# Kernel optimization log

Measured on AMD Instinct MI355X. Metric: run time of the kernel, lower is better.

Reference implementation:

```python
import jax, jax.numpy as jnp
from jax import lax
import numpy as np

N_BITS = 108
N_OUT = 7
# pos_bits[i, j] = bit j (MSB-first) of index i, matching `i >> (6 - j) & 1`
POS_BITS = np.array([[(i >> (6 - j)) & 1 for j in range(N_OUT)] for i in range(N_BITS)], dtype=np.float32)
# LZC value when all 108 bits are zero: 108 = 1101100b, MSB first
LZC_108 = np.array([1, 1, 0, 1, 1, 0, 0], dtype=np.float32)


def setup_inputs() -> dict:
    key = jax.random.key(0)
    # sparse binary bits so leading-zero runs are long and some rows are all-zero
    X = (jax.random.uniform(key, (2_000_000, N_BITS)) < 0.03).astype(jnp.float32)
    return {"X": X}


def _lzd(X):
    """X: [..., 108] MSB-first bits -> [..., 7] LZC MSB-first.

    Arithmetic soft-gate semantics: NOT(a)=1-a, AND(a,b)=a*b,
    OR(a,b)=a+b-a*b, MUX(s,a,b)=s*a+(1-s)*b, OR-tree = 1-prod(1-x).
    Sequential carry over `found` expressed with lax.scan (108 steps).
    """
    batch_shape = X.shape[:-1]
    bits = jnp.moveaxis(X, -1, 0)  # [108, ...]
    pos = jnp.asarray(POS_BITS, dtype=X.dtype)  # [108, 7]

    def step(carry, inp):
        found, lzc = carry                  # found: [..., 1], lzc: [..., 7]
        bit, pos_bits = inp                 # bit: [...], pos_bits: [7]
        bit = bit[..., None]                # [..., 1]
        not_found = 1.0 - found             # NOT
        is_first = bit * not_found          # AND
        # MUX per output bit: is_first ? pos_bit : lzc
        lzc = is_first * pos_bits + (1.0 - is_first) * lzc
        # OR: found | is_first
        found = found + is_first - found * is_first
        return (found, lzc), None

    found0 = jnp.zeros(batch_shape + (1,), X.dtype)
    lzc0 = jnp.zeros(batch_shape + (N_OUT,), X.dtype)
    (found, lzc), _ = lax.scan(step, (found0, lzc0), (bits, pos))

    # OR-tree over all 108 bits, then all-zero override with LZC=108
    any_one = 1.0 - jnp.prod(1.0 - X, axis=-1, keepdims=True)  # [..., 1]
    all_zero = 1.0 - any_one                                   # NOT
    lzc108 = jnp.asarray(LZC_108, dtype=X.dtype)               # [7]
    return all_zero * lzc108 + (1.0 - all_zero) * lzc


def reference(X):
    return _lzd(X)
```

## Files before the change

kernel.cpp:

```cpp
#include <hip/hip_runtime.h>


#define NBITS 108
#define NOUT 7
#define F4R 27

__global__ __launch_bounds__(256) void lzd108_kernel(const uint4* __restrict__ X4,
                                                     float* __restrict__ out,
                                                     int n_rows) {
    const int lane = threadIdx.x & 63;
    const long long wave    = (long long)blockIdx.x * 4 + (threadIdx.x >> 6);
    const long long nwaves  = (long long)gridDim.x * 4;
    const long long ngroups = ((long long)n_rows + 3) >> 2;

    for (long long g = wave; g < ngroups; g += nwaves) {
        const long long row0 = g << 2;
        int rows_here = (int)(n_rows - row0);
        if (rows_here > 4) rows_here = 4;
        const int act0 = (rows_here >= 2 ? 2 : rows_here) * F4R;
        const int act1 = (rows_here > 2 ? rows_here - 2 : 0) * F4R;

        const uint4* base = X4 + row0 * F4R;
        unsigned m0 = 0u, m1 = 0u;
        if (lane < act0) {
            uint4 v = base[lane];
            m0 = (v.x ? 1u : 0u) | (v.y ? 2u : 0u) | (v.z ? 4u : 0u) | (v.w ? 8u : 0u);
        }
        if (lane < act1) {
            uint4 v = base[54 + lane];
            m1 = (v.x ? 1u : 0u) | (v.y ? 2u : 0u) | (v.z ? 4u : 0u) | (v.w ? 8u : 0u);
        }
        const unsigned long long nz0 = __ballot(m0 != 0u);
        const unsigned long long nz1 = __ballot(m1 != 0u);

        int i0 = NBITS, i1 = NBITS, i2 = NBITS, i3 = NBITS;
        {
            const unsigned long long a = nz0 & 0x7FFFFFFull;
            if (a) { const int l = __ffsll(a) - 1;
                     const unsigned mm = __builtin_amdgcn_readlane(m0, l);
                     i0 = l * 4 + __ffs(mm) - 1; }
            const unsigned long long b = (nz0 >> 27) & 0x7FFFFFFull;
            if (b) { const int l = __ffsll(b) - 1;
                     const unsigned mm = __builtin_amdgcn_readlane(m0, l + 27);
                     i1 = l * 4 + __ffs(mm) - 1; }
            const unsigned long long c = nz1 & 0x7FFFFFFull;
            if (c) { const int l = __ffsll(c) - 1;
                     const unsigned mm = __builtin_amdgcn_readlane(m1, l);
                     i2 = l * 4 + __ffs(mm) - 1; }
            const unsigned long long d = (nz1 >> 27) & 0x7FFFFFFull;
            if (d) { const int l = __ffsll(d) - 1;
                     const unsigned mm = __builtin_amdgcn_readlane(m1, l + 27);
                     i3 = l * 4 + __ffs(mm) - 1; }
        }

        if (lane < NOUT * rows_here) {
            const int r = lane / NOUT;
            const int j = lane - r * NOUT;
            const int id01 = (r == 0) ? i0 : i1;
            const int id23 = (r == 2) ? i2 : i3;
            const int id = (r < 2) ? id01 : id23;
            out[row0 * NOUT + lane] = (float)((id >> (6 - j)) & 1);
        }
    }
}

extern "C" void kernel_launch(void* const* d_in, const int* in_sizes, int n_in,
                              void* d_out, int out_size, void* d_ws, size_t ws_size,
                              hipStream_t stream) {
    const uint4* X4 = (const uint4*)d_in[0];
    float* out = (float*)d_out;
    const int n_rows = in_sizes[0] / NBITS;
    const int grid = 4096;
    lzd108_kernel<<<grid, 256, 0, stream>>>(X4, out, n_rows);
}
```

Before: 1.095 ms.

## Scan 8 rows per wave, reading only each row's leading bits first

Each wave now handles 8 rows. It first loads only the first 32 bits (8 uint4) of each row and reads the remaining 76 bits only for rows whose prefix is all zero, batching up to 3 such rows per follow-up load. Because the inputs are sparse, this is meant to skip most of the 432 bytes per row that were previously read, cutting HBM traffic. Outputs are packed and written as float4. The trade-offs are data-dependent branching, serial follow-up loops and scattered partial-row reads that may waste cache-line bandwidth.

```diff
diff --git a/kernel.cpp b/kernel.cpp
--- a/kernel.cpp
+++ b/kernel.cpp
@@ -11,55 +11,99 @@
     const int lane = threadIdx.x & 63;
     const long long wave    = (long long)blockIdx.x * 4 + (threadIdx.x >> 6);
     const long long nwaves  = (long long)gridDim.x * 4;
-    const long long ngroups = ((long long)n_rows + 3) >> 2;
+    const long long ngroups = ((long long)n_rows + 7) >> 3;
+
+    const int r8  = lane >> 3;
+    const int k8  = lane & 7;
+    const int rr  = lane / 19;
+    const int k19 = lane - rr * 19;
 
     for (long long g = wave; g < ngroups; g += nwaves) {
-        const long long row0 = g << 2;
+        const long long row0 = g << 3;
         int rows_here = (int)(n_rows - row0);
-        if (rows_here > 4) rows_here = 4;
-        const int act0 = (rows_here >= 2 ? 2 : rows_here) * F4R;
-        const int act1 = (rows_here > 2 ? rows_here - 2 : 0) * F4R;
+        if (rows_here > 8) rows_here = 8;
+        const uint4* base = X4 + row0 * F4R;
 
-        const uint4* base = X4 + row0 * F4R;
-        unsigned m0 = 0u, m1 = 0u;
-        if (lane < act0) {
-            uint4 v = base[lane];
-            m0 = (v.x ? 1u : 0u) | (v.y ? 2u : 0u) | (v.z ? 4u : 0u) | (v.w ? 8u : 0u);
-        }
-        if (lane < act1) {
-            uint4 v = base[54 + lane];
-            m1 = (v.x ? 1u : 0u) | (v.y ? 2u : 0u) | (v.z ? 4u : 0u) | (v.w ? 8u : 0u);
-        }
-        const unsigned long long nz0 = __ballot(m0 != 0u);
-        const unsigned long long nz1 = __ballot(m1 != 0u);
+        if (rows_here == 8) {
+            uint4 v = base[r8 * F4R + k8];
+            unsigned m = (v.x ? 1u : 0u) | (v.y ? 2u : 0u)
+                       | (v.z ? 4u : 0u) | (v.w ? 8u : 0u);
+            const unsigned long long nz = __ballot(m != 0u);
 
-        int i0 = NBITS, i1 = NBITS, i2 = NBITS, i3 = NBITS;
-        {
-            const unsigned long long a = nz0 & 0x7FFFFFFull;
-            if (a) { const int l = __ffsll(a) - 1;
-                     const unsigned mm = __builtin_amdgcn_readlane(m0, l);
-                     i0 = l * 4 + __ffs(mm) - 1; }
-            const unsigned long long b = (nz0 >> 27) & 0x7FFFFFFull;
-            if (b) { const int l = __ffsll(b) - 1;
-                     const unsigned mm = __builtin_amdgcn_readlane(m0, l + 27);
-                     i1 = l * 4 + __ffs(mm) - 1; }
-            const unsigned long long c = nz1 & 0x7FFFFFFull;
-            if (c) { const int l = __ffsll(c) - 1;
-                     const unsigned mm = __builtin_amdgcn_readlane(m1, l);
-                     i2 = l * 4 + __ffs(mm) - 1; }
-            const unsigned long long d = (nz1 >> 27) & 0x7FFFFFFull;
-            if (d) { const int l = __ffsll(d) - 1;
-                     const unsigned mm = __builtin_amdgcn_readlane(m1, l + 27);
-                     i3 = l * 4 + __ffs(mm) - 1; }
-        }
+            unsigned long long packed = 0;
+            unsigned long long list = 0;
+            int nu = 0;
+            #pragma unroll
+            for (int r = 0; r < 8; ++r) {
+                const unsigned g8 = (unsigned)(nz >> (8 * r)) & 0xFFu;
+                if (g8) {
+                    const int l = __ffs(g8) - 1;
+                    const unsigned mm = __builtin_amdgcn_readlane(m, 8 * r + l);
+                    const unsigned id = 4u * l + __ffs(mm) - 1u;
+                    packed |= (unsigned long long)id << (7 * r);
+                } else {
+                    list |= (unsigned long long)r << (4 * nu);
+                    ++nu;
+                }
+            }
 
-        if (lane < NOUT * rows_here) {
-            const int r = lane / NOUT;
-            const int j = lane - r * NOUT;
-            const int id01 = (r == 0) ? i0 : i1;
-            const int id23 = (r == 2) ? i2 : i3;
-            const int id = (r < 2) ? id01 : id23;
-            out[row0 * NOUT + lane] = (float)((id >> (6 - j)) & 1);
+            int done = 0;
+            while (done < nu) {
+                int take = nu - done;
+                if (take > 3) take = 3;
+                unsigned m2 = 0u;
+                const bool active = (lane < 19 * take);
+                if (active) {
+                    const unsigned rid =
+                        (unsigned)((list >> (4 * (done + rr))) & 0xFull);
+                    uint4 v2 = base[rid * F4R + 8 + k19];
+                    m2 = (v2.x ? 1u : 0u) | (v2.y ? 2u : 0u)
+                       | (v2.z ? 4u : 0u) | (v2.w ? 8u : 0u);
+                }
+                const unsigned long long nz2 = __ballot(m2 != 0u);
+                for (int s = 0; s < take; ++s) {
+                    const unsigned g19 = (unsigned)(nz2 >> (19 * s)) & 0x7FFFFu;
+                    const int r = (int)((list >> (4 * (done + s))) & 0xF);
+                    unsigned id;
+                    if (g19) {
+                        const int l = __ffs(g19) - 1;
+                        const unsigned mm = __builtin_amdgcn_readlane(m2, 19 * s + l);
+                        id = 32u + 4u * l + __ffs(mm) - 1u;
+                    } else {
+                        id = NBITS;
+                    }
+                    packed |= (unsigned long long)id << (7 * r);
+                }
+                done += take;
+            }
+
+            if (lane < 14) {
+                float4 o;
+                float vals[4];
+                #pragma unroll
+                for (int c = 0; c < 4; ++c) {
+                    const int j = 4 * lane + c;
+                    const int row = (j * 9363) >> 16;
+                    const int bit = j - row * NOUT;
+                    const unsigned id = (unsigned)((packed >> (7 * row)) & 0x7Fu);
+                    vals[c] = (float)((id >> (6 - bit)) & 1u);
+                }
+                o.x = vals[0]; o.y = vals[1]; o.z = vals[2]; o.w = vals[3];
+                reinterpret_cast<float4*>(out + row0 * NOUT)[lane] = o;
+            }
+        } else {
+            if (lane < rows_here) {
+                const unsigned* r = reinterpret_cast<const unsigned*>(base)
+                                  + (long long)lane * NBITS;
+                int id = NBITS;
+                for (int j = 0; j < NBITS; ++j) {
+                    if (r[j] != 0u) { id = j; break; }
+                }
+                float* o = out + (row0 + lane) * NOUT;
+                #pragma unroll
+                for (int b = 0; b < NOUT; ++b)
+                    o[b] = (float)((id >> (6 - b)) & 1);
+            }
         }
     }
 }
```

New measurement: 1.057 ms. -3.5%, faster.
